# Optimization experiments

Measured on AMD Instinct MI355X. Metric: run time of the kernel, lower is better.

The kernel has to match this reference:

```python
import jax, jax.numpy as jnp
import numpy as np

# FlowNetC correlation hyperparameters (init_kwargs)
PAD = 4            # pad_size
KERNEL = 1         # kernel_size (1x1 patch)
MD = 4             # max_displacement
STRIDE1 = 1        # stride over output positions
STRIDE2 = 1        # stride over displacements


def setup_inputs() -> dict:
    key = jax.random.key(0)
    k1, k2 = jax.random.split(key)
    input1 = jax.random.normal(k1, (8, 256, 96, 128), dtype=jnp.float32)
    input2 = jax.random.normal(k2, (8, 256, 96, 128), dtype=jnp.float32)
    return {"input1": input1, "input2": input2}


def reference(input1, input2):
    # Cost volume: out[b, d, y, x] = (1/C) * sum_c input1[b,c,y,x] * input2[b,c,y+dy,x+dx]
    # for all displacements (dy, dx) in [-MD, MD] with step STRIDE2.
    # With pad_size == max_displacement, kernel_size == 1, stride1 == 1 the output
    # spatial grid equals the input grid (FlowNetC configuration). Normalization
    # matches correlation_cuda: sumelems = kernel_size^2 * C.
    B, C, H, W = input1.shape
    p2 = jnp.pad(input2, ((0, 0), (0, 0), (PAD, PAD), (PAD, PAD)))
    disp = range(-MD, MD + 1, STRIDE2)  # 9 offsets -> 81 displacement channels
    outs = []
    for dy in disp:
        for dx in disp:
            shifted = jax.lax.dynamic_slice(p2, (0, 0, PAD + dy, PAD + dx), (B, C, H, W))
            # mean over channels == sum / (KERNEL*KERNEL*C) since KERNEL == 1
            outs.append(jnp.mean(input1 * shifted, axis=1))
    return jnp.stack(outs, axis=1)  # [B, 81, H, W]
```

## Files before the change

kernel.cpp:

```cpp
#include <hip/hip_runtime.h>
#include <hip/hip_bf16.h>


#define H_ 96
#define W_ 128
#define HW_ 12288
#define CHW_ 3145728

#define IN2OFF (128 * 64)
#define LDS_BYTES (704 * 64)

typedef __attribute__((ext_vector_type(8))) short short8;
typedef __attribute__((ext_vector_type(4))) float f32x4;

__device__ __forceinline__ int grpswz(int g, int p) {
    return ((g ^ (p & 3) ^ ((p >> 2) & 3)) & 3) * 16;
}

__global__ __launch_bounds__(1024, 4) void corr_mfma3(
    const float* __restrict__ in1,
    const float* __restrict__ in2,
    float* __restrict__ out)
{
    __shared__ __align__(16) char lds[LDS_BYTES];

    const int tid = threadIdx.x;
    const int blk = blockIdx.x;
    const int b   = blk & 7;
    const int i   = blk >> 3;
    const int yt  = i >> 2;
    const int xq  = i & 3;

    const bool stager = (tid < 704);
    const float* gbase = nullptr;
    bool valid = false;
    int lds_dst0 = 0;
    int kk = 0;
    if (stager) {
        if (tid < 576) {
            const int pq = tid % 144;
            const int g  = tid / 144;
            const int r  = pq / 12;
            const int q  = pq % 12;
            const int gx = xq * 32 - 8 + 4 * q;
            const int ry = yt * 4 - 4 + r;
            valid = (ry >= 0) && (ry < H_) && (gx >= 0) && (gx <= W_ - 4);
            gbase = in2 + (size_t)b * CHW_ + (size_t)(8 * g) * HW_ + ry * W_ + gx;
            lds_dst0 = IN2OFF + (r * 48 + 4 * q) * 64;
            kk = g ^ (q & 3);
        } else {
            const int u1 = tid - 576;
            const int pq = u1 % 32;
            const int g  = u1 / 32;
            const int r  = pq / 8;
            const int q  = pq % 8;
            const int gx = xq * 32 + 4 * q;
            const int yy = yt * 4 + r;
            valid = true;
            gbase = in1 + (size_t)b * CHW_ + (size_t)(8 * g) * HW_ + yy * W_ + gx;
            lds_dst0 = (r * 32 + 4 * q) * 64;
            kk = g ^ (q & 3);
        }
    }

    const int lane = tid & 63;
    const int wv   = tid >> 6;
    const int xt   = wv & 1;
    const int ut   = (wv >> 1) & 1;
    const int yp   = wv >> 2;
    const int ln   = lane & 15;
    const int qd   = lane >> 4;

    const int pA   = 16 * xt + ln;
    const int offA = (yp * 32 + pA) * 64 + grpswz(qd, pA);
    const int pB   = 16 * (xt + ut) + ln;
    const int offB = IN2OFF + (yp * 48 + pB) * 64 + grpswz(qd, pB);

    f32x4 acc[9];
    #pragma unroll
    for (int s = 0; s < 9; ++s) acc[s] = f32x4{0.f, 0.f, 0.f, 0.f};

    float4 pf[8];
    #pragma unroll
    for (int j = 0; j < 8; ++j) pf[j] = float4{0.f, 0.f, 0.f, 0.f};
    if (stager && valid) {
        #pragma unroll
        for (int j = 0; j < 8; ++j) pf[j] = *(const float4*)(gbase + (size_t)j * HW_);
    }

    #pragma unroll
    for (int kc = 0; kc < 8; ++kc) {
        if (kc > 0) __syncthreads();
        if (stager) {
            #pragma unroll
            for (int px = 0; px < 4; ++px) {
                union { __hip_bfloat162 h2[4]; short8 s8; } u;
                #pragma unroll
                for (int jj = 0; jj < 4; ++jj) {
                    float2 f;
                    f.x = ((const float*)&pf[2 * jj])[px];
                    f.y = ((const float*)&pf[2 * jj + 1])[px];
                    u.h2[jj] = __float22bfloat162_rn(f);
                }
                *(short8*)(lds + lds_dst0 + px * 64 + ((kk ^ px) & 3) * 16) = u.s8;
            }
        }
        __syncthreads();
        if (kc < 7 && stager) {
            const float* g2 = gbase + (size_t)(32 * (kc + 1)) * HW_;
            #pragma unroll
            for (int j = 0; j < 8; ++j)
                pf[j] = valid ? *(const float4*)(g2 + (size_t)j * HW_)
                              : float4{0.f, 0.f, 0.f, 0.f};
        }
        short8 afr = *(const short8*)(lds + offA);
        #pragma unroll
        for (int s = 0; s < 9; ++s) {
            short8 bfr = *(const short8*)(lds + offB + s * (48 * 64));
            acc[s] = __builtin_amdgcn_mfma_f32_16x16x32_bf16(afr, bfr, acc[s], 0, 0, 0);
        }
    }

    const float scale = 1.0f / 256.0f;
    const int x0 = xq * 32 + 16 * xt;
    const int y  = yt * 4 + yp;
    #pragma unroll
    for (int s = 0; s < 9; ++s) {
        #pragma unroll
        for (int r = 0; r < 4; ++r) {
            const int m  = qd * 4 + r;
            const int dx = ln - m - 8 + 16 * ut;
            if (dx >= -4 && dx <= 4) {
                out[(((size_t)b * 81 + (size_t)(s * 9 + dx + 4)) * H_ + y) * W_ + (x0 + m)]
                    = acc[s][r] * scale;
            }
        }
    }
}

extern "C" void kernel_launch(void* const* d_in, const int* in_sizes, int n_in,
                              void* d_out, int out_size, void* d_ws, size_t ws_size,
                              hipStream_t stream) {
    const float* in1 = (const float*)d_in[0];
    const float* in2 = (const float*)d_in[1];
    float* out = (float*)d_out;

    corr_mfma3<<<768, 1024, 0, stream>>>(in1, in2, out);
}
```

Baseline: 270.6 us.

## Pre-convert input2 to padded bf16 channel-last workspace and drop LDS staging

Adds a pre-pass that converts input2 to bf16 in a zero-padded, channel-interleaved layout in the workspace, so the correlation kernel can load MFMA B fragments directly from global memory without LDS staging or barriers. The new correlation kernel also converts input1 fragments from fp32 in registers per wave. The old single-kernel path is kept as a fallback when the workspace is too small. The trade-off is an extra kernel launch and a write-then-read round trip of about 61 MB of converted data, plus repeated global B loads that rely on L2 for reuse, in exchange for removing LDS traffic and synchronisation.

```diff
diff --git a/kernel.cpp b/kernel.cpp
--- a/kernel.cpp
+++ b/kernel.cpp
@@ -6,80 +6,157 @@
 #define W_ 128
 #define HW_ 12288
 #define CHW_ 3145728
+#define Y2 104
+#define X2 144
+#define ROWB 73728
+#define PLANEB 7667712ULL
+#define WS_NEEDED 61341696ULL
+
+typedef __attribute__((ext_vector_type(8))) short short8;
+typedef __attribute__((ext_vector_type(4))) float f32x4;
+
+__global__ __launch_bounds__(256) void cvt_in2(
+    const float* __restrict__ in2, char* __restrict__ in2t)
+{
+    int idx = blockIdx.x * 256 + threadIdx.x;
+    int px2 = idx % X2;
+    int r   = idx / X2;
+    int cg  = r & 31;
+    r >>= 5;
+    int yp  = r % Y2;
+    int b   = r / Y2;
+
+    short8 v = short8{0, 0, 0, 0, 0, 0, 0, 0};
+    const int gx = px2 - 8, gy = yp - 4;
+    if (gx >= 0 && gx < W_ && gy >= 0 && gy < H_) {
+        const float* sp = in2 + (size_t)b * CHW_ + (size_t)(cg * 8) * HW_
+                              + (size_t)gy * W_ + gx;
+        union { __hip_bfloat162 h2[4]; short8 s8; } u;
+        #pragma unroll
+        for (int j = 0; j < 4; ++j) {
+            float2 f{ sp[(size_t)(2 * j) * HW_], sp[(size_t)(2 * j + 1) * HW_] };
+            u.h2[j] = __float22bfloat162_rn(f);
+        }
+        v = u.s8;
+    }
+    *(short8*)(in2t + (size_t)b * PLANEB + (size_t)yp * ROWB
+                    + (size_t)px2 * 512 + cg * 16) = v;
+}
+
+__global__ __launch_bounds__(512) void corr_pass2(
+    const float* __restrict__ in1,
+    const char*  __restrict__ in2t,
+    float* __restrict__ out)
+{
+    const int tid = threadIdx.x;
+    const int blk = blockIdx.x;
+    const int b   = blk & 7;
+    const int i   = blk >> 3;
+    const int y   = i >> 1;
+    const int xh  = i & 1;
+
+    const int lane = tid & 63;
+    const int wv   = tid >> 6;
+    const int mt   = wv >> 1;
+    const int ut   = wv & 1;
+    const int ln   = lane & 15;
+    const int qd   = lane >> 4;
+    const int x0   = xh * 64 + mt * 16;
+
+    const float* Ab = in1 + (size_t)b * CHW_ + (size_t)(qd * 8) * HW_
+                          + (size_t)y * W_ + (x0 + ln);
+    const int upad = x0 + 16 * ut + ln;
+    const char* Bb = in2t + (size_t)b * PLANEB + (size_t)y * ROWB
+                          + (size_t)upad * 512 + qd * 16;
+
+    f32x4 acc[9];
+    #pragma unroll
+    for (int s = 0; s < 9; ++s) acc[s] = f32x4{0.f, 0.f, 0.f, 0.f};
+
+    #pragma unroll
+    for (int kc = 0; kc < 8; ++kc) {
+        const float* ap = Ab + (size_t)(kc * 32) * HW_;
+        float av[8];
+        #pragma unroll
+        for (int j = 0; j < 8; ++j) av[j] = ap[(size_t)j * HW_];
+        union { __hip_bfloat162 h2[4]; short8 s8; } ua;
+        #pragma unroll
+        for (int j = 0; j < 4; ++j)
+            ua.h2[j] = __float22bfloat162_rn(float2{av[2 * j], av[2 * j + 1]});
+        const short8 afr = ua.s8;
+
+        const char* bp = Bb + kc * 64;
+        #pragma unroll
+        for (int s = 0; s < 9; ++s) {
+            short8 bfr = *(const short8*)(bp + (size_t)s * ROWB);
+            acc[s] = __builtin_amdgcn_mfma_f32_16x16x32_bf16(afr, bfr, acc[s], 0, 0, 0);
+        }
+    }
+
+    const float scale = 1.0f / 256.0f;
+    #pragma unroll
+    for (int s = 0; s < 9; ++s) {
+        #pragma unroll
+        for (int r = 0; r < 4; ++r) {
+            const int m  = qd * 4 + r;
+            const int dx = ln - m - 8 + 16 * ut;
+            if (dx >= -4 && dx <= 4) {
+                out[(((size_t)b * 81 + (size_t)(s * 9 + dx + 4)) * H_ + y) * W_ + (x0 + m)]
+                    = acc[s][r] * scale;
+            }
+        }
+    }
+}
 
 #define IN2OFF (128 * 64)
 #define LDS_BYTES (704 * 64)
-
-typedef __attribute__((ext_vector_type(8))) short short8;
-typedef __attribute__((ext_vector_type(4))) float f32x4;
-
 __device__ __forceinline__ int grpswz(int g, int p) {
     return ((g ^ (p & 3) ^ ((p >> 2) & 3)) & 3) * 16;
 }
-
 __global__ __launch_bounds__(1024, 4) void corr_mfma3(
-    const float* __restrict__ in1,
-    const float* __restrict__ in2,
-    float* __restrict__ out)
+    const float* __restrict__ in1, const float* __restrict__ in2, float* __restrict__ out)
 {
     __shared__ __align__(16) char lds[LDS_BYTES];
-
     const int tid = threadIdx.x;
     const int blk = blockIdx.x;
     const int b   = blk & 7;
     const int i   = blk >> 3;
     const int yt  = i >> 2;
     const int xq  = i & 3;
-
     const bool stager = (tid < 704);
     const float* gbase = nullptr;
     bool valid = false;
-    int lds_dst0 = 0;
-    int kk = 0;
+    int lds_dst0 = 0, kk = 0;
     if (stager) {
         if (tid < 576) {
-            const int pq = tid % 144;
-            const int g  = tid / 144;
-            const int r  = pq / 12;
-            const int q  = pq % 12;
-            const int gx = xq * 32 - 8 + 4 * q;
-            const int ry = yt * 4 - 4 + r;
+            const int pq = tid % 144, g = tid / 144;
+            const int r = pq / 12, q = pq % 12;
+            const int gx = xq * 32 - 8 + 4 * q, ry = yt * 4 - 4 + r;
             valid = (ry >= 0) && (ry < H_) && (gx >= 0) && (gx <= W_ - 4);
             gbase = in2 + (size_t)b * CHW_ + (size_t)(8 * g) * HW_ + ry * W_ + gx;
             lds_dst0 = IN2OFF + (r * 48 + 4 * q) * 64;
             kk = g ^ (q & 3);
         } else {
             const int u1 = tid - 576;
-            const int pq = u1 % 32;
-            const int g  = u1 / 32;
-            const int r  = pq / 8;
-            const int q  = pq % 8;
-            const int gx = xq * 32 + 4 * q;
-            const int yy = yt * 4 + r;
+            const int pq = u1 % 32, g = u1 / 32;
+            const int r = pq / 8, q = pq % 8;
+            const int gx = xq * 32 + 4 * q, yy = yt * 4 + r;
             valid = true;
             gbase = in1 + (size_t)b * CHW_ + (size_t)(8 * g) * HW_ + yy * W_ + gx;
             lds_dst0 = (r * 32 + 4 * q) * 64;
             kk = g ^ (q & 3);
         }
     }
-
-    const int lane = tid & 63;
-    const int wv   = tid >> 6;
-    const int xt   = wv & 1;
-    const int ut   = (wv >> 1) & 1;
-    const int yp   = wv >> 2;
-    const int ln   = lane & 15;
-    const int qd   = lane >> 4;
-
-    const int pA   = 16 * xt + ln;
+    const int lane = tid & 63, wv = tid >> 6;
+    const int xt = wv & 1, ut = (wv >> 1) & 1, yp = wv >> 2;
+    const int ln = lane & 15, qd = lane >> 4;
+    const int pA = 16 * xt + ln;
     const int offA = (yp * 32 + pA) * 64 + grpswz(qd, pA);
-    const int pB   = 16 * (xt + ut) + ln;
+    const int pB = 16 * (xt + ut) + ln;
     const int offB = IN2OFF + (yp * 48 + pB) * 64 + grpswz(qd, pB);
-
     f32x4 acc[9];
     #pragma unroll
     for (int s = 0; s < 9; ++s) acc[s] = f32x4{0.f, 0.f, 0.f, 0.f};
-
     float4 pf[8];
     #pragma unroll
     for (int j = 0; j < 8; ++j) pf[j] = float4{0.f, 0.f, 0.f, 0.f};
@@ -87,7 +164,6 @@
         #pragma unroll
         for (int j = 0; j < 8; ++j) pf[j] = *(const float4*)(gbase + (size_t)j * HW_);
     }
-
     #pragma unroll
     for (int kc = 0; kc < 8; ++kc) {
         if (kc > 0) __syncthreads();
@@ -110,8 +186,7 @@
             const float* g2 = gbase + (size_t)(32 * (kc + 1)) * HW_;
             #pragma unroll
             for (int j = 0; j < 8; ++j)
-                pf[j] = valid ? *(const float4*)(g2 + (size_t)j * HW_)
-                              : float4{0.f, 0.f, 0.f, 0.f};
+                pf[j] = valid ? *(const float4*)(g2 + (size_t)j * HW_) : float4{0.f, 0.f, 0.f, 0.f};
         }
         short8 afr = *(const short8*)(lds + offA);
         #pragma unroll
@@ -120,20 +195,18 @@
             acc[s] = __builtin_amdgcn_mfma_f32_16x16x32_bf16(afr, bfr, acc[s], 0, 0, 0);
         }
     }
-
     const float scale = 1.0f / 256.0f;
     const int x0 = xq * 32 + 16 * xt;
-    const int y  = yt * 4 + yp;
+    const int y = yt * 4 + yp;
     #pragma unroll
     for (int s = 0; s < 9; ++s) {
         #pragma unroll
         for (int r = 0; r < 4; ++r) {
-            const int m  = qd * 4 + r;
+            const int m = qd * 4 + r;
             const int dx = ln - m - 8 + 16 * ut;
-            if (dx >= -4 && dx <= 4) {
+            if (dx >= -4 && dx <= 4)
                 out[(((size_t)b * 81 + (size_t)(s * 9 + dx + 4)) * H_ + y) * W_ + (x0 + m)]
                     = acc[s][r] * scale;
-            }
         }
     }
 }
@@ -145,5 +218,11 @@
     const float* in2 = (const float*)d_in[1];
     float* out = (float*)d_out;
 
-    corr_mfma3<<<768, 1024, 0, stream>>>(in1, in2, out);
-}
+    if (ws_size >= WS_NEEDED) {
+        char* in2t = (char*)d_ws;
+        cvt_in2<<<14976, 256, 0, stream>>>(in2, in2t);
+        corr_pass2<<<1536, 512, 0, stream>>>(in1, in2t, out);
+    } else {
+        corr_mfma3<<<768, 1024, 0, stream>>>(in1, in2, out);
+    }
+}
```

New measurement: 359.6 us. 1.33x slower.
